# Optimization experiments

Measured on AMD Instinct MI355X. Metric: run time of the kernel, lower is better.

Reference implementation:

```python
import jax, jax.numpy as jnp
import numpy as np

N_NODES = 5000
N_EDGES = 160000
HID = 64
NODE_F = 4
TASK_F = 4
BATCH = 512


def _glorot(key, shape):
    fan_in = shape[-1]
    return jax.random.normal(key, shape, dtype=jnp.float32) / jnp.sqrt(jnp.float32(fan_in))


def setup_inputs() -> dict:
    key = jax.random.key(0)
    ks = jax.random.split(key, 16)
    x = jax.random.normal(ks[0], (N_NODES, NODE_F), dtype=jnp.float32)
    edge_index = jax.random.randint(ks[1], (2, N_EDGES), 0, N_NODES, dtype=jnp.int64)
    task_feat = jax.random.normal(ks[2], (BATCH, TASK_F), dtype=jnp.float32)
    return {
        "x": x,
        "edge_index": edge_index,
        "task_feat": task_feat,
        # SAGEConv layer 1: out = lin_l(mean_neigh) + lin_r(x); lin_l has bias, lin_r (root) has no bias (PyG default)
        "Wl1": _glorot(ks[3], (HID, NODE_F)), "bl1": jnp.zeros((HID,), jnp.float32),
        "Wr1": _glorot(ks[4], (HID, NODE_F)),
        # SAGEConv layer 2
        "Wl2": _glorot(ks[5], (HID, HID)), "bl2": jnp.zeros((HID,), jnp.float32),
        "Wr2": _glorot(ks[6], (HID, HID)),
        # task_encoder: Linear(4,64) -> ReLU -> Linear(64,64)
        "Wt1": _glorot(ks[7], (HID, TASK_F)), "bt1": jnp.zeros((HID,), jnp.float32),
        "Wt2": _glorot(ks[8], (HID, HID)), "bt2": jnp.zeros((HID,), jnp.float32),
        # classifier: Linear(128,64) -> ReLU -> Linear(64,1)
        "Wc1": _glorot(ks[9], (HID, 2 * HID)), "bc1": jnp.zeros((HID,), jnp.float32),
        "Wc2": _glorot(ks[10], (1, HID)), "bc2": jnp.zeros((1,), jnp.float32),
    }


def _sage_conv(x, src, dst, Wl, bl, Wr):
    # PyG SAGEConv(mean): messages flow src -> dst; mean over incoming neighbors
    msg_sum = jax.ops.segment_sum(x[src], dst, num_segments=N_NODES)
    deg = jax.ops.segment_sum(jnp.ones((src.shape[0],), x.dtype), dst, num_segments=N_NODES)
    mean_neigh = msg_sum / jnp.maximum(deg, 1.0)[:, None]
    return mean_neigh @ Wl.T + bl + x @ Wr.T


def reference(x, edge_index, task_feat,
              Wl1, bl1, Wr1, Wl2, bl2, Wr2,
              Wt1, bt1, Wt2, bt2, Wc1, bc1, Wc2, bc2):
    src, dst = edge_index[0], edge_index[1]
    h = jax.nn.relu(_sage_conv(x, src, dst, Wl1, bl1, Wr1))        # [N, HID]
    h = jax.nn.relu(_sage_conv(h, src, dst, Wl2, bl2, Wr2))        # [N, HID]
    t = jax.nn.relu(task_feat @ Wt1.T + bt1) @ Wt2.T + bt2         # [B, HID]
    # classifier on concat([h, t]) == split Wc1 into h-part and t-part; avoids materializing the concat
    h_part = h @ Wc1[:, :HID].T                                    # [N, HID]
    t_part = t @ Wc1[:, HID:].T + bc1                              # [B, HID]
    hidden = jax.nn.relu(h_part[None, :, :] + t_part[:, None, :])  # [B, N, HID]
    scores = jnp.einsum('bnh,h->bn', hidden, Wc2[0]) + bc2[0]      # [B, N]
    return scores
```

## Files before the change

### kernel.cpp

```cpp
#include <hip/hip_runtime.h>

#define N_NODES 5000
#define N_EDGES 160000
#define HID 64
#define BATCH 512


__global__ void count_kernel(const int* __restrict__ ei, int* __restrict__ deg) {
    int e = blockIdx.x * 256 + threadIdx.x;
    if (e < N_EDGES) atomicAdd(&deg[ei[N_EDGES + e]], 1);
}

__global__ void scan_kernel(const int* __restrict__ deg, int* __restrict__ row_start) {
    __shared__ int sh[1024];
    __shared__ int s_carry;
    if (threadIdx.x == 0) s_carry = 0;
    __syncthreads();
    for (int base = 0; base < N_NODES; base += 1024) {
        int i = base + (int)threadIdx.x;
        int v = (i < N_NODES) ? deg[i] : 0;
        sh[threadIdx.x] = v;
        __syncthreads();
        for (int off = 1; off < 1024; off <<= 1) {
            int t = (threadIdx.x >= (unsigned)off) ? sh[threadIdx.x - off] : 0;
            __syncthreads();
            sh[threadIdx.x] += t;
            __syncthreads();
        }
        int incl = sh[threadIdx.x];
        int carry = s_carry;
        if (i < N_NODES) row_start[i] = carry + incl - v;
        __syncthreads();
        if (threadIdx.x == 1023) s_carry = carry + sh[1023];
        __syncthreads();
    }
}

__global__ void reorder_kernel(const int* __restrict__ ei, const int* __restrict__ row_start,
                               int* __restrict__ cursor, int* __restrict__ sorted_src) {
    int e = blockIdx.x * 256 + threadIdx.x;
    if (e < N_EDGES) {
        int dst = ei[N_EDGES + e];
        int pos = atomicAdd(&cursor[dst], 1);
        sorted_src[row_start[dst] + pos] = ei[e];
    }
}


__global__ void transpose_kernel(const float* __restrict__ Wl1, const float* __restrict__ Wr1,
                                 const float* __restrict__ Wt1, const float* __restrict__ Wl2,
                                 const float* __restrict__ Wr2, const float* __restrict__ Wt2,
                                 const float* __restrict__ Wc1,
                                 float* __restrict__ Wl1T, float* __restrict__ Wr1T,
                                 float* __restrict__ Wt1T, float* __restrict__ Wl2T,
                                 float* __restrict__ Wr2T, float* __restrict__ Wt2T,
                                 float* __restrict__ Wc1hT, float* __restrict__ Wc1tT) {
    int k = blockIdx.x;
    int h = threadIdx.x;
    Wl2T[k * 64 + h]  = Wl2[h * 64 + k];
    Wr2T[k * 64 + h]  = Wr2[h * 64 + k];
    Wt2T[k * 64 + h]  = Wt2[h * 64 + k];
    Wc1hT[k * 64 + h] = Wc1[h * 128 + k];
    Wc1tT[k * 64 + h] = Wc1[h * 128 + 64 + k];
    if (k < 4) {
        Wl1T[k * 64 + h] = Wl1[h * 4 + k];
        Wr1T[k * 64 + h] = Wr1[h * 4 + k];
        Wt1T[k * 64 + h] = Wt1[h * 4 + k];
    }
}


__global__ __launch_bounds__(64) void layer1_kernel(
        const float* __restrict__ x, const int* __restrict__ deg,
        const int* __restrict__ row_start, const int* __restrict__ sorted_src,
        const float* __restrict__ Wl1T, const float* __restrict__ bl1,
        const float* __restrict__ Wr1T, float* __restrict__ h1) {
    int n = blockIdx.x;
    int lane = threadIdx.x;
    int d = deg[n];
    int s0 = row_start[n];
    int f = lane & 3;
    int g = lane >> 2;
    float acc = 0.f;
    for (int j = g; j < d; j += 16) {
        int s = sorted_src[s0 + j];
        acc += x[s * 4 + f];
    }
    acc += __shfl_down(acc, 32);
    acc += __shfl_down(acc, 16);
    acc += __shfl_down(acc, 8);
    acc += __shfl_down(acc, 4);
    __shared__ float mean[4], xn[4];
    if (lane < 4) {
        mean[lane] = acc / fmaxf((float)d, 1.f);
        xn[lane] = x[n * 4 + lane];
    }
    __syncthreads();
    float v = bl1[lane];
#pragma unroll
    for (int ff = 0; ff < 4; ff++)
        v += mean[ff] * Wl1T[ff * 64 + lane] + xn[ff] * Wr1T[ff * 64 + lane];
    h1[n * 64 + lane] = fmaxf(v, 0.f);
}


__global__ __launch_bounds__(64) void layer2_kernel(
        const float* __restrict__ h1, const int* __restrict__ deg,
        const int* __restrict__ row_start, const int* __restrict__ sorted_src,
        const float* __restrict__ Wl2T, const float* __restrict__ bl2,
        const float* __restrict__ Wr2T, const float* __restrict__ Wc1hT,
        float* __restrict__ h_part) {
    int n = blockIdx.x;
    int h = threadIdx.x;
    int d = deg[n];
    int s0 = row_start[n];
    float a0 = 0.f, a1 = 0.f, a2 = 0.f, a3 = 0.f;
    int j = 0;
    for (; j + 4 <= d; j += 4) {
        int e0 = sorted_src[s0 + j];
        int e1 = sorted_src[s0 + j + 1];
        int e2 = sorted_src[s0 + j + 2];
        int e3 = sorted_src[s0 + j + 3];
        a0 += h1[e0 * 64 + h];
        a1 += h1[e1 * 64 + h];
        a2 += h1[e2 * 64 + h];
        a3 += h1[e3 * 64 + h];
    }
    for (; j < d; j++) a0 += h1[sorted_src[s0 + j] * 64 + h];
    float m = (a0 + a1 + a2 + a3) / fmaxf((float)d, 1.f);

    __shared__ float shm[64], shh[64], shh2[64];
    shm[h] = m;
    shh[h] = h1[n * 64 + h];
    __syncthreads();
    float v = bl2[h];
#pragma unroll
    for (int k = 0; k < 64; k++)
        v += shm[k] * Wl2T[k * 64 + h] + shh[k] * Wr2T[k * 64 + h];
    float h2v = fmaxf(v, 0.f);
    shh2[h] = h2v;
    __syncthreads();
    float p = 0.f;
#pragma unroll
    for (int k = 0; k < 64; k++) p += shh2[k] * Wc1hT[k * 64 + h];
    h_part[n * 64 + h] = p;
}


__global__ __launch_bounds__(64) void task_kernel(
        const float* __restrict__ task_feat,
        const float* __restrict__ Wt1T, const float* __restrict__ bt1,
        const float* __restrict__ Wt2T, const float* __restrict__ bt2,
        const float* __restrict__ Wc1tT, const float* __restrict__ bc1,
        float* __restrict__ t_part) {
    int b = blockIdx.x;
    int h = threadIdx.x;
    __shared__ float s1[64], s2[64];
    float t0 = task_feat[b * 4 + 0];
    float t1 = task_feat[b * 4 + 1];
    float t2 = task_feat[b * 4 + 2];
    float t3 = task_feat[b * 4 + 3];
    float v = bt1[h] + t0 * Wt1T[h] + t1 * Wt1T[64 + h] + t2 * Wt1T[128 + h] + t3 * Wt1T[192 + h];
    s1[h] = fmaxf(v, 0.f);
    __syncthreads();
    float v2 = bt2[h];
#pragma unroll
    for (int k = 0; k < 64; k++) v2 += s1[k] * Wt2T[k * 64 + h];
    s2[h] = v2;
    __syncthreads();
    float p = bc1[h];
#pragma unroll
    for (int k = 0; k < 64; k++) p += s2[k] * Wc1tT[k * 64 + h];
    t_part[b * 64 + h] = p;
}


__global__ __launch_bounds__(256) void scores_kernel(
        const float* __restrict__ h_part, const float* __restrict__ t_part,
        const float* __restrict__ Wc2, const float* __restrict__ bc2,
        float* __restrict__ out) {
    int tid = threadIdx.x;
    int n = blockIdx.x * 256 + tid;
    bool valid = n < N_NODES;
    int nn = valid ? n : (N_NODES - 1);
    float hr[64];
    const float4* hp = (const float4*)(h_part + nn * 64);
#pragma unroll
    for (int i = 0; i < 16; i++) {
        float4 v = hp[i];
        hr[4 * i + 0] = v.x; hr[4 * i + 1] = v.y;
        hr[4 * i + 2] = v.z; hr[4 * i + 3] = v.w;
    }
    float b2 = bc2[0];
    int b0 = blockIdx.y * 16;
    for (int bb = 0; bb < 16; bb++) {
        const float* tp = t_part + (b0 + bb) * 64;
        float acc = 0.f;
#pragma unroll
        for (int h = 0; h < 64; h++)
            acc = fmaf(fmaxf(hr[h] + tp[h], 0.f), Wc2[h], acc);
        if (valid) out[(b0 + bb) * N_NODES + n] = acc + b2;
    }
}


extern "C" void kernel_launch(void* const* d_in, const int* in_sizes, int n_in,
                              void* d_out, int out_size, void* d_ws, size_t ws_size,
                              hipStream_t stream) {
    const float* x    = (const float*)d_in[0];
    const int*   ei   = (const int*)d_in[1];
    const float* task = (const float*)d_in[2];
    const float* Wl1  = (const float*)d_in[3];
    const float* bl1  = (const float*)d_in[4];
    const float* Wr1  = (const float*)d_in[5];
    const float* Wl2  = (const float*)d_in[6];
    const float* bl2  = (const float*)d_in[7];
    const float* Wr2  = (const float*)d_in[8];
    const float* Wt1  = (const float*)d_in[9];
    const float* bt1  = (const float*)d_in[10];
    const float* Wt2  = (const float*)d_in[11];
    const float* bt2  = (const float*)d_in[12];
    const float* Wc1  = (const float*)d_in[13];
    const float* bc1  = (const float*)d_in[14];
    const float* Wc2  = (const float*)d_in[15];
    const float* bc2  = (const float*)d_in[16];
    float* out = (float*)d_out;

    char* ws = (char*)d_ws;
    int*   deg        = (int*)(ws + 0);
    int*   cursor     = (int*)(ws + 20000);
    int*   row_start  = (int*)(ws + 40064);
    int*   sorted_src = (int*)(ws + 60160);
    float* h1         = (float*)(ws + 700416);
    float* h_part     = (float*)(ws + 1980672);
    float* t_part     = (float*)(ws + 3260928);
    float* Wl1T  = (float*)(ws + 3392256);
    float* Wr1T  = (float*)(ws + 3393280);
    float* Wt1T  = (float*)(ws + 3394304);
    float* Wl2T  = (float*)(ws + 3395328);
    float* Wr2T  = (float*)(ws + 3411712);
    float* Wt2T  = (float*)(ws + 3428096);
    float* Wc1hT = (float*)(ws + 3444480);
    float* Wc1tT = (float*)(ws + 3460864);

    hipMemsetAsync(ws, 0, 40000, stream);

    transpose_kernel<<<64, 64, 0, stream>>>(Wl1, Wr1, Wt1, Wl2, Wr2, Wt2, Wc1,
                                            Wl1T, Wr1T, Wt1T, Wl2T, Wr2T, Wt2T,
                                            Wc1hT, Wc1tT);
    count_kernel<<<(N_EDGES + 255) / 256, 256, 0, stream>>>(ei, deg);
    scan_kernel<<<1, 1024, 0, stream>>>(deg, row_start);
    reorder_kernel<<<(N_EDGES + 255) / 256, 256, 0, stream>>>(ei, row_start, cursor, sorted_src);
    layer1_kernel<<<N_NODES, 64, 0, stream>>>(x, deg, row_start, sorted_src, Wl1T, bl1, Wr1T, h1);
    layer2_kernel<<<N_NODES, 64, 0, stream>>>(h1, deg, row_start, sorted_src, Wl2T, bl2, Wr2T,
                                              Wc1hT, h_part);
    task_kernel<<<BATCH, 64, 0, stream>>>(task, Wt1T, bt1, Wt2T, bt2, Wc1tT, bc1, t_part);
    scores_kernel<<<dim3(20, 32), 256, 0, stream>>>(h_part, t_part, Wc2, bc2, out);
}
```

Measured before the change: 169.2 us.

## Fuse prep, scatter layer-1 aggregation via atomics, warp-shuffle scan, batch nodes per block

Replaces the memset, transpose and task kernels with one prep kernel that zeroes the workspace, transposes the weights and computes the task encoder with float4 reads. Layer 1 now sums neighbor features with float atomics during the degree count, so it no longer gathers through the sorted CSR. The single-block scan becomes a per-thread serial scan plus wave shuffles and runs in the same launch as the layer-1 epilogue. Layer 2 processes four nodes per 256-thread block. This cuts launch count and serialization; float atomics make layer-1 sums order-nondeterministic.

```diff
diff --git a/kernel.cpp b/kernel.cpp
--- a/kernel.cpp
+++ b/kernel.cpp
@@ -6,38 +6,134 @@
 #define BATCH 512
 
 
-__global__ void count_kernel(const int* __restrict__ ei, int* __restrict__ deg) {
+__global__ __launch_bounds__(64) void prep_kernel(
+        const float* __restrict__ Wl1, const float* __restrict__ Wr1,
+        const float* __restrict__ Wl2, const float* __restrict__ Wr2,
+        const float* __restrict__ Wc1,
+        const float* __restrict__ task_feat,
+        const float* __restrict__ Wt1, const float* __restrict__ bt1,
+        const float* __restrict__ Wt2, const float* __restrict__ bt2,
+        const float* __restrict__ bc1,
+        int* __restrict__ zero_region,
+        float* __restrict__ Wl1T, float* __restrict__ Wr1T,
+        float* __restrict__ Wl2T, float* __restrict__ Wr2T,
+        float* __restrict__ Wc1hT, float* __restrict__ t_part) {
+    int h = threadIdx.x;
+    if (blockIdx.x < 64) {
+        int k = blockIdx.x;
+        int gtid = k * 64 + h;
+#pragma unroll
+        for (int r = 0; r < 8; r++) {
+            int idx = r * 4096 + gtid;
+            if (idx < 30000) zero_region[idx] = 0;
+        }
+        Wl2T[k * 64 + h]  = Wl2[h * 64 + k];
+        Wr2T[k * 64 + h]  = Wr2[h * 64 + k];
+        Wc1hT[k * 64 + h] = Wc1[h * 128 + k];
+        if (k < 4) {
+            Wl1T[k * 64 + h] = Wl1[h * 4 + k];
+            Wr1T[k * 64 + h] = Wr1[h * 4 + k];
+        }
+    } else {
+        int b = blockIdx.x - 64;
+        __shared__ float s1[64], s2[64];
+        float4 tf = ((const float4*)task_feat)[b];
+        float4 w1 = ((const float4*)Wt1)[h];
+        float v = bt1[h] + tf.x * w1.x + tf.y * w1.y + tf.z * w1.z + tf.w * w1.w;
+        s1[h] = fmaxf(v, 0.f);
+        __syncthreads();
+        const float4* w2r = (const float4*)(Wt2 + h * 64);
+        const float4* s1v = (const float4*)s1;
+        float v2 = bt2[h];
+#pragma unroll
+        for (int q = 0; q < 16; q++) {
+            float4 w = w2r[q]; float4 s = s1v[q];
+            v2 += s.x * w.x + s.y * w.y + s.z * w.z + s.w * w.w;
+        }
+        s2[h] = v2;
+        __syncthreads();
+        const float4* wc = (const float4*)(Wc1 + h * 128 + 64);
+        const float4* s2v = (const float4*)s2;
+        float p = bc1[h];
+#pragma unroll
+        for (int q = 0; q < 16; q++) {
+            float4 w = wc[q]; float4 s = s2v[q];
+            p += s.x * w.x + s.y * w.y + s.z * w.z + s.w * w.w;
+        }
+        t_part[b * 64 + h] = p;
+    }
+}
+
+__global__ __launch_bounds__(256) void scatter_kernel(
+        const int* __restrict__ ei, const float* __restrict__ x,
+        int* __restrict__ deg, float* __restrict__ xsum) {
     int e = blockIdx.x * 256 + threadIdx.x;
-    if (e < N_EDGES) atomicAdd(&deg[ei[N_EDGES + e]], 1);
-}
-
-__global__ void scan_kernel(const int* __restrict__ deg, int* __restrict__ row_start) {
-    __shared__ int sh[1024];
-    __shared__ int s_carry;
-    if (threadIdx.x == 0) s_carry = 0;
-    __syncthreads();
-    for (int base = 0; base < N_NODES; base += 1024) {
-        int i = base + (int)threadIdx.x;
-        int v = (i < N_NODES) ? deg[i] : 0;
-        sh[threadIdx.x] = v;
+    if (e >= N_EDGES) return;
+    int src = ei[e];
+    int dst = ei[N_EDGES + e];
+    atomicAdd(&deg[dst], 1);
+    float4 v = ((const float4*)x)[src];
+    atomicAdd(&xsum[dst * 4 + 0], v.x);
+    atomicAdd(&xsum[dst * 4 + 1], v.y);
+    atomicAdd(&xsum[dst * 4 + 2], v.z);
+    atomicAdd(&xsum[dst * 4 + 3], v.w);
+}
+
+__global__ __launch_bounds__(256) void scan_layer1_kernel(
+        const int* __restrict__ deg, const float* __restrict__ xsum,
+        const float* __restrict__ x,
+        const float* __restrict__ Wl1T, const float* __restrict__ bl1,
+        const float* __restrict__ Wr1T,
+        int* __restrict__ row_start, float* __restrict__ h1) {
+    if (blockIdx.x == 0) {
+        int t = threadIdx.x;
+        int lane = t & 63, wave = t >> 6;
+        int vals[20];
+        int tot = 0;
+        int base_i = t * 20;
+#pragma unroll
+        for (int j = 0; j < 20; j++) {
+            int idx = base_i + j;
+            int dv = (idx < N_NODES) ? deg[idx] : 0;
+            vals[j] = tot;
+            tot += dv;
+        }
+        int scan = tot;
+#pragma unroll
+        for (int off = 1; off < 64; off <<= 1) {
+            int nb = __shfl_up(scan, off);
+            if (lane >= off) scan += nb;
+        }
+        __shared__ int wtot[4];
+        if (lane == 63) wtot[wave] = scan;
         __syncthreads();
-        for (int off = 1; off < 1024; off <<= 1) {
-            int t = (threadIdx.x >= (unsigned)off) ? sh[threadIdx.x - off] : 0;
-            __syncthreads();
-            sh[threadIdx.x] += t;
-            __syncthreads();
-        }
-        int incl = sh[threadIdx.x];
-        int carry = s_carry;
-        if (i < N_NODES) row_start[i] = carry + incl - v;
-        __syncthreads();
-        if (threadIdx.x == 1023) s_carry = carry + sh[1023];
-        __syncthreads();
-    }
-}
-
-__global__ void reorder_kernel(const int* __restrict__ ei, const int* __restrict__ row_start,
-                               int* __restrict__ cursor, int* __restrict__ sorted_src) {
+        int wbase = 0;
+        for (int w = 0; w < wave; w++) wbase += wtot[w];
+        int tbase = wbase + scan - tot;
+#pragma unroll
+        for (int j = 0; j < 20; j++) {
+            int idx = base_i + j;
+            if (idx < N_NODES) row_start[idx] = tbase + vals[j];
+        }
+    } else {
+        int lane = threadIdx.x & 63;
+        int n = (blockIdx.x - 1) * 4 + (threadIdx.x >> 6);
+        int d = deg[n];
+        float inv = 1.f / fmaxf((float)d, 1.f);
+        float4 xs = ((const float4*)xsum)[n];
+        float4 xv = ((const float4*)x)[n];
+        float v = bl1[lane]
+                + (xs.x * inv) * Wl1T[0 * 64 + lane] + xv.x * Wr1T[0 * 64 + lane]
+                + (xs.y * inv) * Wl1T[1 * 64 + lane] + xv.y * Wr1T[1 * 64 + lane]
+                + (xs.z * inv) * Wl1T[2 * 64 + lane] + xv.z * Wr1T[2 * 64 + lane]
+                + (xs.w * inv) * Wl1T[3 * 64 + lane] + xv.w * Wr1T[3 * 64 + lane];
+        h1[n * 64 + lane] = fmaxf(v, 0.f);
+    }
+}
+
+__global__ __launch_bounds__(256) void reorder_kernel(
+        const int* __restrict__ ei, const int* __restrict__ row_start,
+        int* __restrict__ cursor, int* __restrict__ sorted_src) {
     int e = blockIdx.x * 256 + threadIdx.x;
     if (e < N_EDGES) {
         int dst = ei[N_EDGES + e];
@@ -46,72 +142,15 @@
     }
 }
 
-
-__global__ void transpose_kernel(const float* __restrict__ Wl1, const float* __restrict__ Wr1,
-                                 const float* __restrict__ Wt1, const float* __restrict__ Wl2,
-                                 const float* __restrict__ Wr2, const float* __restrict__ Wt2,
-                                 const float* __restrict__ Wc1,
-                                 float* __restrict__ Wl1T, float* __restrict__ Wr1T,
-                                 float* __restrict__ Wt1T, float* __restrict__ Wl2T,
-                                 float* __restrict__ Wr2T, float* __restrict__ Wt2T,
-                                 float* __restrict__ Wc1hT, float* __restrict__ Wc1tT) {
-    int k = blockIdx.x;
-    int h = threadIdx.x;
-    Wl2T[k * 64 + h]  = Wl2[h * 64 + k];
-    Wr2T[k * 64 + h]  = Wr2[h * 64 + k];
-    Wt2T[k * 64 + h]  = Wt2[h * 64 + k];
-    Wc1hT[k * 64 + h] = Wc1[h * 128 + k];
-    Wc1tT[k * 64 + h] = Wc1[h * 128 + 64 + k];
-    if (k < 4) {
-        Wl1T[k * 64 + h] = Wl1[h * 4 + k];
-        Wr1T[k * 64 + h] = Wr1[h * 4 + k];
-        Wt1T[k * 64 + h] = Wt1[h * 4 + k];
-    }
-}
-
-
-__global__ __launch_bounds__(64) void layer1_kernel(
-        const float* __restrict__ x, const int* __restrict__ deg,
-        const int* __restrict__ row_start, const int* __restrict__ sorted_src,
-        const float* __restrict__ Wl1T, const float* __restrict__ bl1,
-        const float* __restrict__ Wr1T, float* __restrict__ h1) {
-    int n = blockIdx.x;
-    int lane = threadIdx.x;
-    int d = deg[n];
-    int s0 = row_start[n];
-    int f = lane & 3;
-    int g = lane >> 2;
-    float acc = 0.f;
-    for (int j = g; j < d; j += 16) {
-        int s = sorted_src[s0 + j];
-        acc += x[s * 4 + f];
-    }
-    acc += __shfl_down(acc, 32);
-    acc += __shfl_down(acc, 16);
-    acc += __shfl_down(acc, 8);
-    acc += __shfl_down(acc, 4);
-    __shared__ float mean[4], xn[4];
-    if (lane < 4) {
-        mean[lane] = acc / fmaxf((float)d, 1.f);
-        xn[lane] = x[n * 4 + lane];
-    }
-    __syncthreads();
-    float v = bl1[lane];
-#pragma unroll
-    for (int ff = 0; ff < 4; ff++)
-        v += mean[ff] * Wl1T[ff * 64 + lane] + xn[ff] * Wr1T[ff * 64 + lane];
-    h1[n * 64 + lane] = fmaxf(v, 0.f);
-}
-
-
-__global__ __launch_bounds__(64) void layer2_kernel(
+__global__ __launch_bounds__(256) void layer2_kernel(
         const float* __restrict__ h1, const int* __restrict__ deg,
         const int* __restrict__ row_start, const int* __restrict__ sorted_src,
         const float* __restrict__ Wl2T, const float* __restrict__ bl2,
         const float* __restrict__ Wr2T, const float* __restrict__ Wc1hT,
         float* __restrict__ h_part) {
-    int n = blockIdx.x;
-    int h = threadIdx.x;
+    int h = threadIdx.x & 63;
+    int grp = threadIdx.x >> 6;
+    int n = blockIdx.x * 4 + grp;
     int d = deg[n];
     int s0 = row_start[n];
     float a0 = 0.f, a1 = 0.f, a2 = 0.f, a3 = 0.f;
@@ -129,51 +168,21 @@
     for (; j < d; j++) a0 += h1[sorted_src[s0 + j] * 64 + h];
     float m = (a0 + a1 + a2 + a3) / fmaxf((float)d, 1.f);
 
-    __shared__ float shm[64], shh[64], shh2[64];
-    shm[h] = m;
-    shh[h] = h1[n * 64 + h];
+    __shared__ float shm[4][64], shh[4][64], shh2[4][64];
+    shm[grp][h] = m;
+    shh[grp][h] = h1[n * 64 + h];
     __syncthreads();
     float v = bl2[h];
 #pragma unroll
     for (int k = 0; k < 64; k++)
-        v += shm[k] * Wl2T[k * 64 + h] + shh[k] * Wr2T[k * 64 + h];
-    float h2v = fmaxf(v, 0.f);
-    shh2[h] = h2v;
+        v += shm[grp][k] * Wl2T[k * 64 + h] + shh[grp][k] * Wr2T[k * 64 + h];
+    shh2[grp][h] = fmaxf(v, 0.f);
     __syncthreads();
     float p = 0.f;
 #pragma unroll
-    for (int k = 0; k < 64; k++) p += shh2[k] * Wc1hT[k * 64 + h];
+    for (int k = 0; k < 64; k++) p += shh2[grp][k] * Wc1hT[k * 64 + h];
     h_part[n * 64 + h] = p;
 }
-
-
-__global__ __launch_bounds__(64) void task_kernel(
-        const float* __restrict__ task_feat,
-        const float* __restrict__ Wt1T, const float* __restrict__ bt1,
-        const float* __restrict__ Wt2T, const float* __restrict__ bt2,
-        const float* __restrict__ Wc1tT, const float* __restrict__ bc1,
-        float* __restrict__ t_part) {
-    int b = blockIdx.x;
-    int h = threadIdx.x;
-    __shared__ float s1[64], s2[64];
-    float t0 = task_feat[b * 4 + 0];
-    float t1 = task_feat[b * 4 + 1];
-    float t2 = task_feat[b * 4 + 2];
-    float t3 = task_feat[b * 4 + 3];
-    float v = bt1[h] + t0 * Wt1T[h] + t1 * Wt1T[64 + h] + t2 * Wt1T[128 + h] + t3 * Wt1T[192 + h];
-    s1[h] = fmaxf(v, 0.f);
-    __syncthreads();
-    float v2 = bt2[h];
-#pragma unroll
-    for (int k = 0; k < 64; k++) v2 += s1[k] * Wt2T[k * 64 + h];
-    s2[h] = v2;
-    __syncthreads();
-    float p = bc1[h];
-#pragma unroll
-    for (int k = 0; k < 64; k++) p += s2[k] * Wc1tT[k * 64 + h];
-    t_part[b * 64 + h] = p;
-}
-
 
 __global__ __launch_bounds__(256) void scores_kernel(
         const float* __restrict__ h_part, const float* __restrict__ t_part,
@@ -202,7 +211,6 @@
         if (valid) out[(b0 + bb) * N_NODES + n] = acc + b2;
     }
 }
-
 
 extern "C" void kernel_launch(void* const* d_in, const int* in_sizes, int n_in,
                               void* d_out, int out_size, void* d_ws, size_t ws_size,
@@ -229,31 +237,28 @@
     char* ws = (char*)d_ws;
     int*   deg        = (int*)(ws + 0);
     int*   cursor     = (int*)(ws + 20000);
-    int*   row_start  = (int*)(ws + 40064);
-    int*   sorted_src = (int*)(ws + 60160);
-    float* h1         = (float*)(ws + 700416);
-    float* h_part     = (float*)(ws + 1980672);
-    float* t_part     = (float*)(ws + 3260928);
-    float* Wl1T  = (float*)(ws + 3392256);
-    float* Wr1T  = (float*)(ws + 3393280);
-    float* Wt1T  = (float*)(ws + 3394304);
-    float* Wl2T  = (float*)(ws + 3395328);
-    float* Wr2T  = (float*)(ws + 3411712);
-    float* Wt2T  = (float*)(ws + 3428096);
-    float* Wc1hT = (float*)(ws + 3444480);
-    float* Wc1tT = (float*)(ws + 3460864);
-
-    hipMemsetAsync(ws, 0, 40000, stream);
-
-    transpose_kernel<<<64, 64, 0, stream>>>(Wl1, Wr1, Wt1, Wl2, Wr2, Wt2, Wc1,
-                                            Wl1T, Wr1T, Wt1T, Wl2T, Wr2T, Wt2T,
-                                            Wc1hT, Wc1tT);
-    count_kernel<<<(N_EDGES + 255) / 256, 256, 0, stream>>>(ei, deg);
-    scan_kernel<<<1, 1024, 0, stream>>>(deg, row_start);
+    float* xsum       = (float*)(ws + 40000);
+    int*   zero_reg   = (int*)(ws + 0);
+    int*   row_start  = (int*)(ws + 120000);
+    int*   sorted_src = (int*)(ws + 140000);
+    float* h1         = (float*)(ws + 780000);
+    float* h_part     = (float*)(ws + 2060000);
+    float* t_part     = (float*)(ws + 3340000);
+    float* Wl1T  = (float*)(ws + 3471072);
+    float* Wr1T  = (float*)(ws + 3472096);
+    float* Wl2T  = (float*)(ws + 3473120);
+    float* Wr2T  = (float*)(ws + 3489504);
+    float* Wc1hT = (float*)(ws + 3505888);
+
+    prep_kernel<<<64 + BATCH, 64, 0, stream>>>(Wl1, Wr1, Wl2, Wr2, Wc1,
+                                               task, Wt1, bt1, Wt2, bt2, bc1,
+                                               zero_reg, Wl1T, Wr1T, Wl2T, Wr2T,
+                                               Wc1hT, t_part);
+    scatter_kernel<<<(N_EDGES + 255) / 256, 256, 0, stream>>>(ei, x, deg, xsum);
+    scan_layer1_kernel<<<1 + N_NODES / 4, 256, 0, stream>>>(deg, xsum, x, Wl1T, bl1, Wr1T,
+                                                            row_start, h1);
     reorder_kernel<<<(N_EDGES + 255) / 256, 256, 0, stream>>>(ei, row_start, cursor, sorted_src);
-    layer1_kernel<<<N_NODES, 64, 0, stream>>>(x, deg, row_start, sorted_src, Wl1T, bl1, Wr1T, h1);
-    layer2_kernel<<<N_NODES, 64, 0, stream>>>(h1, deg, row_start, sorted_src, Wl2T, bl2, Wr2T,
-                                              Wc1hT, h_part);
-    task_kernel<<<BATCH, 64, 0, stream>>>(task, Wt1T, bt1, Wt2T, bt2, Wc1tT, bc1, t_part);
+    layer2_kernel<<<N_NODES / 4, 256, 0, stream>>>(h1, deg, row_start, sorted_src,
+                                                   Wl2T, bl2, Wr2T, Wc1hT, h_part);
     scores_kernel<<<dim3(20, 32), 256, 0, stream>>>(h_part, t_part, Wc2, bc2, out);
 }
```

Result: slower. 204.0 us (+20.6%).
